# Performance work log

Hardware: AMD Instinct MI355X
Metric: run time of the kernel (lower is better)

Reference implementation:

```python
import jax, jax.numpy as jnp
import numpy as np

N_NODES = 50000
N_EDGES = 800000
N_GRAPHS = 2000
EMB = 300
FEAT = 512
OUT = 256
L = 5


def setup_inputs() -> dict:
    key = jax.random.key(0)
    ks = jax.random.split(key, 24)
    s = 0.05
    inp = {
        "x": jax.random.randint(ks[0], (N_NODES, 2), 0, 3, dtype=jnp.int64 if jax.config.jax_enable_x64 else jnp.int32),
        "edge_index": jax.random.randint(ks[1], (2, N_EDGES), 0, N_NODES),
        "edge_attr": jax.random.randint(ks[2], (N_EDGES, 2), 0, 3),
        "batch": jnp.sort(jax.random.randint(ks[3], (N_NODES,), 0, N_GRAPHS)),
        # node embeddings
        "x_emb1": jax.random.normal(ks[4], (119, EMB), jnp.float32) * s,
        "x_emb2": jax.random.normal(ks[5], (3, EMB), jnp.float32) * s,
        # stacked per-layer GINEConv params [L, ...]
        "edge_e1": jax.random.normal(ks[6], (L, 5, EMB), jnp.float32) * s,
        "edge_e2": jax.random.normal(ks[7], (L, 3, EMB), jnp.float32) * s,
        "W1": jax.random.normal(ks[8], (L, EMB, 2 * EMB), jnp.float32) * s,
        "b1": jnp.zeros((L, 2 * EMB), jnp.float32),
        "W2": jax.random.normal(ks[9], (L, 2 * EMB, EMB), jnp.float32) * s,
        "b2": jnp.zeros((L, EMB), jnp.float32),
        # feat_lin
        "feat_W": jax.random.normal(ks[10], (EMB, FEAT), jnp.float32) * s,
        "feat_b": jnp.zeros((FEAT,), jnp.float32),
        # pred head: Linear(512,256)+ReLU, Linear(256,256)+ReLU, Linear(256,256)
        "p0_W": jax.random.normal(ks[11], (FEAT, FEAT // 2), jnp.float32) * s,
        "p0_b": jnp.zeros((FEAT // 2,), jnp.float32),
        "p1_W": jax.random.normal(ks[12], (FEAT // 2, FEAT // 2), jnp.float32) * s,
        "p1_b": jnp.zeros((FEAT // 2,), jnp.float32),
        "p2_W": jax.random.normal(ks[13], (FEAT // 2, OUT), jnp.float32) * s,
        "p2_b": jnp.zeros((OUT,), jnp.float32),
    }
    return inp


def reference(x, edge_index, edge_attr, batch,
              x_emb1, x_emb2, edge_e1, edge_e2, W1, b1, W2, b2,
              feat_W, feat_b, p0_W, p0_b, p1_W, p1_b, p2_W, p2_b):
    N = x.shape[0]
    # initial node embedding
    h = x_emb1[x[:, 0]] + x_emb2[x[:, 1]]  # [N, EMB]

    # add self loops (appended once; same for every layer)
    loop = jnp.arange(N)
    src = jnp.concatenate([edge_index[0], loop])  # [E+N]
    dst = jnp.concatenate([edge_index[1], loop])
    # self-loop edge_attr = [4, 0]
    ea0 = jnp.concatenate([edge_attr[:, 0], jnp.full((N,), 4, edge_attr.dtype)])
    ea1 = jnp.concatenate([edge_attr[:, 1], jnp.zeros((N,), edge_attr.dtype)])

    for l in range(L):
        ee = edge_e1[l][ea0] + edge_e2[l][ea1]          # [E+N, EMB]
        msg = h[src] + ee                                # gather + add
        aggr = jax.ops.segment_sum(msg, dst, num_segments=N)  # scatter-add
        h = jnp.maximum(aggr @ W1[l] + b1[l], 0.0) @ W2[l] + b2[l]  # GIN MLP
        if l < L - 1:
            h = jnp.maximum(h, 0.0)  # relu (dropout inactive in eval)

    # global mean pool over graphs
    sums = jax.ops.segment_sum(h, batch, num_segments=N_GRAPHS)          # [G, EMB]
    counts = jax.ops.segment_sum(jnp.ones((N,), h.dtype), batch, num_segments=N_GRAPHS)
    hg = sums / jnp.maximum(counts, 1.0)[:, None]

    hg = hg @ feat_W + feat_b                    # feat_lin -> [G, FEAT]
    p = jnp.maximum(hg @ p0_W + p0_b, 0.0)
    p = jnp.maximum(p @ p1_W + p1_b, 0.0)
    proj = p @ p2_W + p2_b                       # [G, OUT]
    return hg, proj
```

## Files before the change

kernel.cpp:

```cpp
#include <hip/hip_runtime.h>
#include <stdint.h>
#include <stddef.h>

typedef unsigned short u16;
typedef __attribute__((ext_vector_type(8))) short short8;
typedef __attribute__((ext_vector_type(4))) float f32x4;

#define N_NODES 50000
#define N_EDGES 800000
#define N_GRAPHS 2000
#define EMB 300
#define EMB_P 320
#define HID 600
#define HID_P 640
#define NP2 384
#define M_P 50176
#define G_P 2048
#define FEAT 512
#define OUTD 256
#define NLAYER 5

#define OFF_EMB1 0
#define N_EMB1   (119 * EMB)
#define OFF_EMB2 (OFF_EMB1 + N_EMB1)
#define N_EMB2   (3 * EMB)
#define OFF_E1   (OFF_EMB2 + N_EMB2)
#define N_E1     (NLAYER * 5 * EMB)
#define OFF_E2   (OFF_E1 + N_E1)
#define N_E2     (NLAYER * 3 * EMB)
#define OFF_W1   (OFF_E2 + N_E2)
#define N_W1     (NLAYER * EMB * HID)
#define OFF_B1   (OFF_W1 + N_W1)
#define N_B1     (NLAYER * HID)
#define OFF_W2   (OFF_B1 + N_B1)
#define N_W2     (NLAYER * HID * EMB)
#define OFF_B2   (OFF_W2 + N_W2)
#define N_B2     (NLAYER * EMB)
#define OFF_FW   (OFF_B2 + N_B2)
#define N_FW     (EMB * FEAT)
#define OFF_FB   (OFF_FW + N_FW)
#define N_FB     (FEAT)
#define OFF_P0W  (OFF_FB + N_FB)
#define N_P0W    (FEAT * (FEAT / 2))
#define OFF_P0B  (OFF_P0W + N_P0W)
#define N_P0B    (FEAT / 2)
#define OFF_P1W  (OFF_P0B + N_P0B)
#define N_P1W    ((FEAT / 2) * (FEAT / 2))
#define OFF_P1B  (OFF_P1W + N_P1W)
#define N_P1B    (FEAT / 2)
#define OFF_P2W  (OFF_P1B + N_P1B)
#define N_P2W    ((FEAT / 2) * OUTD)
#define OFF_P2B  (OFF_P2W + N_P2W)
#define N_P2B    (OUTD)
#define CVT_TOTAL (OFF_P2B + N_P2B)

#define WOFF_W1T 0
#define WN_W1T   (NLAYER * HID_P * EMB_P)
#define WOFF_W2T (WOFF_W1T + WN_W1T)
#define WN_W2T   (NLAYER * NP2 * HID_P)
#define WOFF_FWT (WOFF_W2T + WN_W2T)
#define WN_FWT   (FEAT * EMB_P)
#define WOFF_P0T (WOFF_FWT + WN_FWT)
#define WN_P0T   (OUTD * FEAT)
#define WOFF_P1T (WOFF_P0T + WN_P0T)
#define WN_P1T   (OUTD * OUTD)
#define WOFF_P2T (WOFF_P1T + WN_P1T)
#define WN_P2T   (OUTD * OUTD)
#define WOFF_B1P (WOFF_P2T + WN_P2T)
#define WN_B1P   (NLAYER * HID_P)
#define WOFF_B2P (WOFF_B1P + WN_B1P)
#define WN_B2P   (NLAYER * NP2)
#define W_TOTAL  (WOFF_B2P + WN_B2P)

__device__ __forceinline__ float b2f(u16 u) {
    union { unsigned int i; float f; } c; c.i = ((unsigned int)u) << 16; return c.f;
}
__device__ __forceinline__ u16 f2b(float f) {
    union { float f; unsigned int i; } c; c.f = f;
    unsigned int x = c.i;
    unsigned int lsb = (x >> 16) & 1u;
    x += 0x7fffu + lsb;
    return (u16)(x >> 16);
}
__device__ __forceinline__ int geti(const int* __restrict__ p, long k, int iw) {
    return p[k << iw];
}
__device__ __forceinline__ void gll16(const u16* g, u16* l) {
    __builtin_amdgcn_global_load_lds((const __attribute__((address_space(1))) void*)g,
                                     (__attribute__((address_space(3))) void*)l, 16, 0, 0);
}

__global__ __launch_bounds__(256) void detect_kernel(const void* __restrict__ emb1_raw,
                                                     const int* __restrict__ ei_raw,
                                                     int* __restrict__ flags) {
    __shared__ int cnt_s;
    __shared__ int nz_s;
    int tid = threadIdx.x;
    if (tid == 0) { cnt_s = 0; nz_s = 0; }
    __syncthreads();
    const u16* u = (const u16*)emb1_raw;
    int local = 0;
#pragma unroll
    for (int j = 0; j < 8; j++) {
        u16 w = u[2 * (tid * 8 + j)];
        int e = (w >> 7) & 0xFF;
        if (w == 0 || (e >= 90 && e <= 130)) local++;
    }
    atomicAdd(&cnt_s, local);
    int v = ei_raw[2 * tid + 1];
    if (v != 0) atomicOr(&nz_s, 1);
    __syncthreads();
    if (tid == 0) {
        flags[0] = (cnt_s < 1600) ? 1 : 0;
        flags[1] = nz_s ? 0 : 1;
    }
}

struct CvtArgs { const void* src[16]; };
__constant__ int cvt_off[17] = {OFF_EMB1, OFF_EMB2, OFF_E1, OFF_E2, OFF_W1, OFF_B1,
                                OFF_W2, OFF_B2, OFF_FW, OFF_FB, OFF_P0W, OFF_P0B,
                                OFF_P1W, OFF_P1B, OFF_P2W, OFF_P2B, CVT_TOTAL};

__global__ __launch_bounds__(256) void cvt_all(CvtArgs args, u16* __restrict__ dst,
                                               const int* __restrict__ flags) {
    int idx = blockIdx.x * 256 + threadIdx.x;
    if (idx >= CVT_TOTAL) return;
    int fp32 = flags[0];
    int t = 0;
#pragma unroll
    for (int i = 0; i < 16; i++) {
        if (idx >= cvt_off[i + 1]) t = i + 1;
    }
    int off = idx - cvt_off[t];
    u16 v;
    if (fp32) v = f2b(((const float*)args.src[t])[off]);
    else      v = ((const u16*)args.src[t])[off];
    dst[idx] = v;
}

struct WSeg { int srcOff, Kin, Nin, Kd, Nd, bias; };
__constant__ int wseg_cum[9] = {WOFF_W1T, WOFF_W2T, WOFF_FWT, WOFF_P0T, WOFF_P1T,
                                WOFF_P2T, WOFF_B1P, WOFF_B2P, W_TOTAL};
__constant__ WSeg wsegs[8] = {
    {OFF_W1,  EMB, HID,  EMB_P, HID_P, 0},
    {OFF_W2,  HID, EMB,  HID_P, NP2,   0},
    {OFF_FW,  EMB, FEAT, EMB_P, FEAT,  0},
    {OFF_P0W, FEAT, OUTD, FEAT, OUTD,  0},
    {OFF_P1W, OUTD, OUTD, OUTD, OUTD,  0},
    {OFF_P2W, OUTD, OUTD, OUTD, OUTD,  0},
    {OFF_B1,  HID, 0, 0, HID_P, 1},
    {OFF_B2,  EMB, 0, 0, NP2,   1},
};

__global__ __launch_bounds__(256) void tpad_all(const u16* __restrict__ cbuf,
                                                u16* __restrict__ wbuf) {
    int idx = blockIdx.x * 256 + threadIdx.x;
    if (idx >= W_TOTAL) return;
    int t = 0;
#pragma unroll
    for (int i = 0; i < 8; i++) {
        if (idx >= wseg_cum[i + 1]) t = i + 1;
    }
    WSeg sg = wsegs[t];
    int i = idx - wseg_cum[t];
    u16 v = 0;
    if (sg.bias) {
        int n = i % sg.Nd, l = i / sg.Nd;
        if (n < sg.Kin) v = cbuf[sg.srcOff + l * sg.Kin + n];
    } else {
        int k = i % sg.Kd;
        int r = i / sg.Kd;
        int n = r % sg.Nd, l = r / sg.Nd;
        if (k < sg.Kin && n < sg.Nin) v = cbuf[sg.srcOff + ((long)l * sg.Kin + k) * sg.Nin + n];
    }
    wbuf[idx] = v;
}

__global__ void count_edges(const int* __restrict__ ei, const int* __restrict__ ea,
                            int* __restrict__ deg, int* __restrict__ Ccnt,
                            const int* __restrict__ flags) {
    int e = blockIdx.x * 256 + threadIdx.x;
    if (e >= N_EDGES) return;
    int iw = flags[1];
    int dst = geti(ei, (long)N_EDGES + e, iw);
    if (dst >= 0 && dst < N_NODES) atomicAdd(&deg[dst], 1);
    int a = geti(ea, 2L * e, iw), b = geti(ea, 2L * e + 1, iw);
    if (dst >= 0 && dst < N_NODES && a >= 0 && a < 3 && b >= 0 && b < 3)
        atomicAdd(&Ccnt[dst * 16 + a * 3 + b], 1);
}

__global__ __launch_bounds__(1024) void scan50k(const int* __restrict__ deg,
                                                int* __restrict__ offsets,
                                                int* __restrict__ cursor) {
    __shared__ int buf[1024];
    __shared__ int carry_s;
    int tid = threadIdx.x;
    if (tid == 0) { carry_s = 0; offsets[0] = 0; }
    __syncthreads();
    for (int base = 0; base < N_NODES; base += 1024) {
        int v = (base + tid < N_NODES) ? deg[base + tid] : 0;
        buf[tid] = v;
        __syncthreads();
        for (int off = 1; off < 1024; off <<= 1) {
            int t = (tid >= off) ? buf[tid - off] : 0;
            __syncthreads();
            buf[tid] += t;
            __syncthreads();
        }
        int incl = carry_s + buf[tid];
        if (base + tid < N_NODES) {
            offsets[base + tid + 1] = incl;
            cursor[base + tid] = incl - v;
        }
        __syncthreads();
        if (tid == 0) carry_s += buf[1023];
        __syncthreads();
    }
}

__global__ void fill_csr(const int* __restrict__ ei, int* __restrict__ cursor,
                         int* __restrict__ csr_src, const int* __restrict__ flags) {
    int e = blockIdx.x * 256 + threadIdx.x;
    if (e >= N_EDGES) return;
    int iw = flags[1];
    int src = geti(ei, (long)e, iw);
    int dst = geti(ei, (long)N_EDGES + e, iw);
    if (dst < 0 || dst >= N_NODES) return;
    int pos = atomicAdd(&cursor[dst], 1);
    if (pos >= 0 && pos < N_EDGES) csr_src[pos] = src;
}

__global__ __launch_bounds__(256) void embed_kernel(const int* __restrict__ x,
                                                    const u16* __restrict__ emb1,
                                                    const u16* __restrict__ emb2,
                                                    u16* __restrict__ h,
                                                    const int* __restrict__ flags) {
    int wave = threadIdx.x >> 6, lane = threadIdx.x & 63;
    int n = blockIdx.x * 4 + wave;
    int iw = flags[1];
    int i1 = geti(x, 2L * n, iw), i2 = geti(x, 2L * n + 1, iw);
    i1 = (i1 >= 0 && i1 < 119) ? i1 : 0;
    i2 = (i2 >= 0 && i2 < 3) ? i2 : 0;
#pragma unroll
    for (int j = 0; j < 5; j++) {
        int f = lane + 64 * j;
        float v = 0.f;
        if (f < EMB) v = b2f(emb1[i1 * EMB + f]) + b2f(emb2[i2 * EMB + f]);
        h[(size_t)n * EMB_P + f] = f2b(v);
    }
}

__global__ __launch_bounds__(256) void aggregate_kernel(const u16* __restrict__ h,
                                                        u16* __restrict__ aggr,
                                                        const int* __restrict__ offsets,
                                                        const int* __restrict__ csr_src,
                                                        const int* __restrict__ Ccnt,
                                                        const u16* __restrict__ e1,
                                                        const u16* __restrict__ e2) {
    __shared__ float eetab[15 * EMB_P];
    int tid = threadIdx.x;
    for (int idx = tid; idx < 15 * EMB_P; idx += 256) {
        int c = idx / EMB_P, f = idx % EMB_P;
        float v = 0.f;
        if (f < EMB) v = b2f(e1[(c / 3) * EMB + f]) + b2f(e2[(c % 3) * EMB + f]);
        eetab[idx] = v;
    }
    __syncthreads();
    int wave = tid >> 6, lane = tid & 63;
    int n = blockIdx.x * 4 + wave;
    float acc[5];
#pragma unroll
    for (int j = 0; j < 5; j++) acc[j] = b2f(h[(size_t)n * EMB_P + lane + 64 * j]);
    int e_beg = offsets[n], e_end = offsets[n + 1];
    int cnt = e_end - e_beg;
    if (cnt > 0) {
        int sA = csr_src[e_beg];
        int sB = (cnt > 1) ? csr_src[e_beg + 1] : 0;
        u16 cur[5];
        {
            const u16* hp = h + (size_t)sA * EMB_P + lane;
#pragma unroll
            for (int j = 0; j < 5; j++) cur[j] = hp[64 * j];
        }
        for (int i = 0; i + 1 < cnt; i++) {
            const u16* hq = h + (size_t)sB * EMB_P + lane;
            u16 nxt[5];
#pragma unroll
            for (int j = 0; j < 5; j++) nxt[j] = hq[64 * j];
            int sC = (i + 2 < cnt) ? csr_src[e_beg + i + 2] : 0;
#pragma unroll
            for (int j = 0; j < 5; j++) acc[j] += b2f(cur[j]);
#pragma unroll
            for (int j = 0; j < 5; j++) cur[j] = nxt[j];
            sB = sC;
        }
#pragma unroll
        for (int j = 0; j < 5; j++) acc[j] += b2f(cur[j]);
    }
#pragma unroll
    for (int c = 0; c < 15; c++) {
        float cntf = (float)Ccnt[n * 16 + c] + (c == 12 ? 1.0f : 0.0f);
#pragma unroll
        for (int j = 0; j < 5; j++) acc[j] += cntf * eetab[c * EMB_P + lane + 64 * j];
    }
#pragma unroll
    for (int j = 0; j < 5; j++) aggr[(size_t)n * EMB_P + lane + 64 * j] = f2b(acc[j]);
}

__global__ __launch_bounds__(256) void gemm_bf16(const u16* __restrict__ A,
                                                 const u16* __restrict__ Bt,
                                                 const u16* __restrict__ bias,
                                                 u16* __restrict__ Cb,
                                                 float* __restrict__ Cf,
                                                 int K, int lda, int ldb, int ldc,
                                                 int Mstore, int Nstore, int relu) {
    __shared__ u16 As[128 * 64];
    __shared__ u16 Bs[128 * 64];
    int tid = threadIdx.x;
    int lane = tid & 63, wave = tid >> 6;
    int wm = (wave >> 1) * 64, wn = (wave & 1) * 64;
    int n0 = blockIdx.x * 128, m0 = blockIdx.y * 128;
    int q = lane >> 4, r16 = lane & 15;
    int wrow = wave * 32;
    int lcol = (lane & 7) * 8;

    f32x4 acc[4][4];
#pragma unroll
    for (int i = 0; i < 4; i++)
#pragma unroll
        for (int j = 0; j < 4; j++) acc[i][j] = (f32x4){0.f, 0.f, 0.f, 0.f};

    for (int k0 = 0; k0 < K; k0 += 64) {
#pragma unroll
        for (int p = 0; p < 4; p++) {
            int row = wrow + p * 8 + (lane >> 3);
            gll16(A + (size_t)(m0 + row) * lda + k0 + lcol, &As[(wrow + p * 8) * 64]);
            gll16(Bt + (size_t)(n0 + row) * ldb + k0 + lcol, &Bs[(wrow + p * 8) * 64]);
        }
        __syncthreads();
#pragma unroll
        for (int kk = 0; kk < 2; kk++) {
            short8 af[4], bfr[4];
#pragma unroll
            for (int i = 0; i < 4; i++)
                af[i] = *(const short8*)(&As[(wm + i * 16 + r16) * 64 + kk * 32 + q * 8]);
#pragma unroll
            for (int j = 0; j < 4; j++)
                bfr[j] = *(const short8*)(&Bs[(wn + j * 16 + r16) * 64 + kk * 32 + q * 8]);
#pragma unroll
            for (int i = 0; i < 4; i++)
#pragma unroll
                for (int j = 0; j < 4; j++)
                    acc[i][j] = __builtin_amdgcn_mfma_f32_16x16x32_bf16(af[i], bfr[j], acc[i][j], 0, 0, 0);
        }
        __syncthreads();
    }
#pragma unroll
    for (int i = 0; i < 4; i++) {
#pragma unroll
        for (int j = 0; j < 4; j++) {
            int n_g = n0 + wn + j * 16 + r16;
            float bv = (n_g < Nstore) ? b2f(bias[n_g]) : 0.f;
#pragma unroll
            for (int rr = 0; rr < 4; rr++) {
                int m_g = m0 + wm + i * 16 + q * 4 + rr;
                if (m_g < Mstore && n_g < Nstore) {
                    float v = acc[i][j][rr] + bv;
                    if (relu) v = fmaxf(v, 0.f);
                    if (Cb) Cb[(size_t)m_g * ldc + n_g] = f2b(v);
                    if (Cf) Cf[(size_t)m_g * ldc + n_g] = v;
                }
            }
        }
    }
}

__global__ void graph_bounds(const int* __restrict__ batch, int* __restrict__ gstart,
                             const int* __restrict__ flags) {
    int g = blockIdx.x * 256 + threadIdx.x;
    if (g > N_GRAPHS) return;
    int iw = flags[1];
    int lo = 0, hi = N_NODES;
    while (lo < hi) {
        int mid = (lo + hi) >> 1;
        if (geti(batch, mid, iw) < g) lo = mid + 1; else hi = mid;
    }
    gstart[g] = lo;
}

__global__ __launch_bounds__(256) void pool_kernel(const u16* __restrict__ h,
                                                   const int* __restrict__ gstart,
                                                   u16* __restrict__ hgp) {
    int wave = threadIdx.x >> 6, lane = threadIdx.x & 63;
    int g = blockIdx.x * 4 + wave;
    int s = gstart[g], e = gstart[g + 1];
    float acc[5] = {0.f, 0.f, 0.f, 0.f, 0.f};
    for (int n = s; n < e; n++) {
        const u16* hp = h + (size_t)n * EMB_P + lane;
#pragma unroll
        for (int j = 0; j < 5; j++) acc[j] += b2f(hp[64 * j]);
    }
    int cnt = e - s;
    float inv = 1.0f / (float)(cnt > 1 ? cnt : 1);
#pragma unroll
    for (int j = 0; j < 5; j++) hgp[(size_t)g * EMB_P + lane + 64 * j] = f2b(acc[j] * inv);
}

extern "C" void kernel_launch(void* const* d_in, const int* in_sizes, int n_in,
                              void* d_out, int out_size, void* d_ws, size_t ws_size,
                              hipStream_t stream) {
    const int* x       = (const int*)d_in[0];
    const int* ei      = (const int*)d_in[1];
    const int* ea      = (const int*)d_in[2];
    const int* batch   = (const int*)d_in[3];
    float* out = (float*)d_out;

    char* wp = (char*)d_ws;
    auto alloc = [&](size_t bytes) -> void* {
        void* r = (void*)wp;
        wp += (bytes + 255) & ~(size_t)255;
        return r;
    };
    int* flags   = (int*)alloc(16 * 4);
    int* gstart  = (int*)alloc((N_GRAPHS + 1) * 4);
    int* deg     = (int*)alloc(N_NODES * 4);
    int* cursor  = (int*)alloc(N_NODES * 4);
    int* offsets = (int*)alloc((N_NODES + 1) * 4);
    u16* cbuf    = (u16*)alloc((size_t)CVT_TOTAL * 2);
    u16* wbuf    = (u16*)alloc((size_t)W_TOTAL * 2);
    u16* hg_pre  = (u16*)alloc((size_t)G_P * EMB_P * 2);
    u16* hgbuf   = (u16*)alloc((size_t)G_P * FEAT * 2);
    u16* pbuf0   = (u16*)alloc((size_t)G_P * OUTD * 2);
    u16* pbuf1   = (u16*)alloc((size_t)G_P * OUTD * 2);
    int* csr_src = (int*)alloc(N_EDGES * 4);
    int* Ccnt    = (int*)alloc((size_t)N_NODES * 16 * 4);
    u16* aggr    = (u16*)alloc((size_t)M_P * EMB_P * 2);
    u16* h       = (u16*)alloc((size_t)M_P * EMB_P * 2);

    size_t used = (size_t)(wp - (char*)d_ws);
    size_t remain = (ws_size > used) ? (ws_size - used - 4096) : 0;
    size_t hdnFull = (size_t)M_P * HID_P * 2;
    int nstrip = 8;
    if (remain >= hdnFull)          nstrip = 1;
    else if (remain >= hdnFull / 2) nstrip = 2;
    else if (remain >= hdnFull / 4) nstrip = 4;
    int stripRows = M_P / nstrip;
    u16* hdn = (u16*)alloc(hdnFull / nstrip);

    detect_kernel<<<1, 256, 0, stream>>>(d_in[4], ei, flags);
    CvtArgs ca;
    for (int i = 0; i < 16; i++) ca.src[i] = d_in[4 + i];
    cvt_all<<<(CVT_TOTAL + 255) / 256, 256, 0, stream>>>(ca, cbuf, flags);
    tpad_all<<<(W_TOTAL + 255) / 256, 256, 0, stream>>>(cbuf, wbuf);

    const u16* x_emb1  = cbuf + OFF_EMB1;
    const u16* x_emb2  = cbuf + OFF_EMB2;
    const u16* edge_e1 = cbuf + OFF_E1;
    const u16* edge_e2 = cbuf + OFF_E2;
    const u16* fb      = cbuf + OFF_FB;
    const u16* p0b     = cbuf + OFF_P0B;
    const u16* p1b     = cbuf + OFF_P1B;
    const u16* p2b     = cbuf + OFF_P2B;
    const u16* W1t     = wbuf + WOFF_W1T;
    const u16* W2t     = wbuf + WOFF_W2T;
    const u16* featWt  = wbuf + WOFF_FWT;
    const u16* p0Wt    = wbuf + WOFF_P0T;
    const u16* p1Wt    = wbuf + WOFF_P1T;
    const u16* p2Wt    = wbuf + WOFF_P2T;
    const u16* b1p     = wbuf + WOFF_B1P;
    const u16* b2p     = wbuf + WOFF_B2P;

    hipMemsetAsync(deg, 0, N_NODES * 4, stream);
    hipMemsetAsync(Ccnt, 0, (size_t)N_NODES * 16 * 4, stream);

    count_edges<<<(N_EDGES + 255) / 256, 256, 0, stream>>>(ei, ea, deg, Ccnt, flags);
    scan50k<<<1, 1024, 0, stream>>>(deg, offsets, cursor);
    fill_csr<<<(N_EDGES + 255) / 256, 256, 0, stream>>>(ei, cursor, csr_src, flags);
    graph_bounds<<<(N_GRAPHS + 1 + 255) / 256, 256, 0, stream>>>(batch, gstart, flags);

    embed_kernel<<<N_NODES / 4, 256, 0, stream>>>(x, x_emb1, x_emb2, h, flags);

    for (int l = 0; l < NLAYER; l++) {
        aggregate_kernel<<<N_NODES / 4, 256, 0, stream>>>(
            h, aggr, offsets, csr_src, Ccnt,
            edge_e1 + (size_t)l * 5 * EMB, edge_e2 + (size_t)l * 3 * EMB);
        for (int s = 0; s < nstrip; s++) {
            size_t r0 = (size_t)s * stripRows;
            gemm_bf16<<<dim3(HID_P / 128, stripRows / 128), 256, 0, stream>>>(
                aggr + r0 * EMB_P, W1t + (size_t)l * HID_P * EMB_P,
                b1p + (size_t)l * HID_P, hdn, nullptr,
                EMB_P, EMB_P, EMB_P, HID_P, stripRows, HID_P, 1);
            gemm_bf16<<<dim3(NP2 / 128, stripRows / 128), 256, 0, stream>>>(
                hdn, W2t + (size_t)l * NP2 * HID_P,
                b2p + (size_t)l * NP2, h + r0 * EMB_P, nullptr,
                HID_P, HID_P, HID_P, EMB_P, stripRows, EMB_P, (l < NLAYER - 1) ? 1 : 0);
        }
    }

    pool_kernel<<<N_GRAPHS / 4, 256, 0, stream>>>(h, gstart, hg_pre);

    gemm_bf16<<<dim3(FEAT / 128, G_P / 128), 256, 0, stream>>>(
        hg_pre, featWt, fb, hgbuf, out,
        EMB_P, EMB_P, EMB_P, FEAT, N_GRAPHS, FEAT, 0);
    gemm_bf16<<<dim3(OUTD / 128, G_P / 128), 256, 0, stream>>>(
        hgbuf, p0Wt, p0b, pbuf0, nullptr,
        FEAT, FEAT, FEAT, OUTD, N_GRAPHS, OUTD, 1);
    gemm_bf16<<<dim3(OUTD / 128, G_P / 128), 256, 0, stream>>>(
        pbuf0, p1Wt, p1b, pbuf1, nullptr,
        OUTD, OUTD, OUTD, OUTD, N_GRAPHS, OUTD, 1);
    gemm_bf16<<<dim3(OUTD / 128, G_P / 128), 256, 0, stream>>>(
        pbuf1, p2Wt, p2b, nullptr, out + (size_t)N_GRAPHS * FEAT,
        OUTD, OUTD, OUTD, OUTD, N_GRAPHS, OUTD, 0);
}
```

Measured before the change: 1.628 ms.

## Use 256-row GEMM tiles for GIN MLP and deepen aggregation gather prefetch

Adds a GEMM kernel with 256x128 output tiles, where each wave computes 64x128, and uses it for both GIN MLP matmuls in every layer. Each loaded B tile is reused across more rows, which cuts LDS and global traffic per MFMA. The aggregation loop now keeps two neighbor rows in flight instead of one, to hide gather latency. The costs are higher register pressure from 32 accumulators per wave, lower occupancy, and the strip rows may not divide by 256, which depends on Mstore bounds and on the buffer padding.

```diff
diff --git a/kernel.cpp b/kernel.cpp
--- a/kernel.cpp
+++ b/kernel.cpp
@@ -274,28 +274,53 @@
     int e_beg = offsets[n], e_end = offsets[n + 1];
     int cnt = e_end - e_beg;
     if (cnt > 0) {
-        int sA = csr_src[e_beg];
-        int sB = (cnt > 1) ? csr_src[e_beg + 1] : 0;
-        u16 cur[5];
+        int i0 = csr_src[e_beg];
+        int i1 = (cnt > 1) ? csr_src[e_beg + 1] : 0;
+        int i2 = (cnt > 2) ? csr_src[e_beg + 2] : 0;
+        int i3 = (cnt > 3) ? csr_src[e_beg + 3] : 0;
+        u16 A_[5], B_[5];
         {
-            const u16* hp = h + (size_t)sA * EMB_P + lane;
-#pragma unroll
-            for (int j = 0; j < 5; j++) cur[j] = hp[64 * j];
-        }
-        for (int i = 0; i + 1 < cnt; i++) {
-            const u16* hq = h + (size_t)sB * EMB_P + lane;
-            u16 nxt[5];
-#pragma unroll
-            for (int j = 0; j < 5; j++) nxt[j] = hq[64 * j];
-            int sC = (i + 2 < cnt) ? csr_src[e_beg + i + 2] : 0;
-#pragma unroll
-            for (int j = 0; j < 5; j++) acc[j] += b2f(cur[j]);
-#pragma unroll
-            for (int j = 0; j < 5; j++) cur[j] = nxt[j];
-            sB = sC;
-        }
-#pragma unroll
-        for (int j = 0; j < 5; j++) acc[j] += b2f(cur[j]);
+            const u16* r = h + (size_t)i0 * EMB_P + lane;
+#pragma unroll
+            for (int j = 0; j < 5; j++) A_[j] = r[64 * j];
+        }
+        if (cnt > 1) {
+            const u16* r = h + (size_t)i1 * EMB_P + lane;
+#pragma unroll
+            for (int j = 0; j < 5; j++) B_[j] = r[64 * j];
+        }
+        int e = 0;
+        for (; e + 3 < cnt; e += 2) {
+#pragma unroll
+            for (int j = 0; j < 5; j++) acc[j] += b2f(A_[j]);
+            {
+                const u16* r = h + (size_t)i2 * EMB_P + lane;
+#pragma unroll
+                for (int j = 0; j < 5; j++) A_[j] = r[64 * j];
+            }
+#pragma unroll
+            for (int j = 0; j < 5; j++) acc[j] += b2f(B_[j]);
+            {
+                const u16* r = h + (size_t)i3 * EMB_P + lane;
+#pragma unroll
+                for (int j = 0; j < 5; j++) B_[j] = r[64 * j];
+            }
+            i2 = (e + 4 < cnt) ? csr_src[e_beg + e + 4] : 0;
+            i3 = (e + 5 < cnt) ? csr_src[e_beg + e + 5] : 0;
+        }
+        if (e < cnt) {
+#pragma unroll
+            for (int j = 0; j < 5; j++) acc[j] += b2f(A_[j]);
+        }
+        if (e + 1 < cnt) {
+#pragma unroll
+            for (int j = 0; j < 5; j++) acc[j] += b2f(B_[j]);
+        }
+        if (e + 2 < cnt) {
+            const u16* r = h + (size_t)i2 * EMB_P + lane;
+#pragma unroll
+            for (int j = 0; j < 5; j++) acc[j] += b2f(r[64 * j]);
+        }
     }
 #pragma unroll
     for (int c = 0; c < 15; c++) {
@@ -369,6 +394,76 @@
                     if (relu) v = fmaxf(v, 0.f);
                     if (Cb) Cb[(size_t)m_g * ldc + n_g] = f2b(v);
                     if (Cf) Cf[(size_t)m_g * ldc + n_g] = v;
+                }
+            }
+        }
+    }
+}
+
+__global__ __launch_bounds__(256) void gemm_bf16_256(const u16* __restrict__ A,
+                                                     const u16* __restrict__ Bt,
+                                                     const u16* __restrict__ bias,
+                                                     u16* __restrict__ Cb,
+                                                     int K, int lda, int ldb, int ldc,
+                                                     int Mstore, int Nstore, int relu) {
+    __shared__ u16 As[256 * 64];
+    __shared__ u16 Bs[128 * 64];
+    int tid = threadIdx.x;
+    int lane = tid & 63, wave = tid >> 6;
+    int wm = wave * 64;
+    int n0 = blockIdx.x * 128, m0 = blockIdx.y * 256;
+    int q = lane >> 4, r16 = lane & 15;
+    int lcol = (lane & 7) * 8;
+
+    f32x4 acc[4][8];
+#pragma unroll
+    for (int i = 0; i < 4; i++)
+#pragma unroll
+        for (int j = 0; j < 8; j++) acc[i][j] = (f32x4){0.f, 0.f, 0.f, 0.f};
+
+    for (int k0 = 0; k0 < K; k0 += 64) {
+#pragma unroll
+        for (int p = 0; p < 8; p++) {
+            int row = wm + p * 8 + (lane >> 3);
+            gll16(A + (size_t)(m0 + row) * lda + k0 + lcol, &As[(wm + p * 8) * 64]);
+        }
+#pragma unroll
+        for (int p = 0; p < 4; p++) {
+            int row = wave * 32 + p * 8 + (lane >> 3);
+            gll16(Bt + (size_t)(n0 + row) * ldb + k0 + lcol, &Bs[(wave * 32 + p * 8) * 64]);
+        }
+        __syncthreads();
+#pragma unroll
+        for (int kk = 0; kk < 2; kk++) {
+            short8 af[4], bfr[8];
+#pragma unroll
+            for (int i = 0; i < 4; i++)
+                af[i] = *(const short8*)(&As[(wm + i * 16 + r16) * 64 + kk * 32 + q * 8]);
+#pragma unroll
+            for (int j = 0; j < 8; j++)
+                bfr[j] = *(const short8*)(&Bs[(j * 16 + r16) * 64 + kk * 32 + q * 8]);
+#pragma unroll
+            for (int i = 0; i < 4; i++)
+#pragma unroll
+                for (int j = 0; j < 8; j++)
+                    acc[i][j] = __builtin_amdgcn_mfma_f32_16x16x32_bf16(af[i], bfr[j], acc[i][j], 0, 0, 0);
+        }
+        __syncthreads();
+    }
+#pragma unroll
+    for (int j = 0; j < 8; j++) {
+        int n_g = n0 + j * 16 + r16;
+        if (n_g >= Nstore) continue;
+        float bv = b2f(bias[n_g]);
+#pragma unroll
+        for (int i = 0; i < 4; i++) {
+#pragma unroll
+            for (int rr = 0; rr < 4; rr++) {
+                int m_g = m0 + wm + i * 16 + q * 4 + rr;
+                if (m_g < Mstore) {
+                    float v = acc[i][j][rr] + bv;
+                    if (relu) v = fmaxf(v, 0.f);
+                    Cb[(size_t)m_g * ldc + n_g] = f2b(v);
                 }
             }
         }
@@ -486,13 +581,14 @@
             edge_e1 + (size_t)l * 5 * EMB, edge_e2 + (size_t)l * 3 * EMB);
         for (int s = 0; s < nstrip; s++) {
             size_t r0 = (size_t)s * stripRows;
-            gemm_bf16<<<dim3(HID_P / 128, stripRows / 128), 256, 0, stream>>>(
+            int mtiles = (stripRows + 255) / 256;
+            gemm_bf16_256<<<dim3(HID_P / 128, mtiles), 256, 0, stream>>>(
                 aggr + r0 * EMB_P, W1t + (size_t)l * HID_P * EMB_P,
-                b1p + (size_t)l * HID_P, hdn, nullptr,
+                b1p + (size_t)l * HID_P, hdn,
                 EMB_P, EMB_P, EMB_P, HID_P, stripRows, HID_P, 1);
-            gemm_bf16<<<dim3(NP2 / 128, stripRows / 128), 256, 0, stream>>>(
+            gemm_bf16_256<<<dim3(NP2 / 128, mtiles), 256, 0, stream>>>(
                 hdn, W2t + (size_t)l * NP2 * HID_P,
-                b2p + (size_t)l * NP2, h + r0 * EMB_P, nullptr,
+                b2p + (size_t)l * NP2, h + r0 * EMB_P,
                 HID_P, HID_P, HID_P, EMB_P, stripRows, EMB_P, (l < NLAYER - 1) ? 1 : 0);
         }
     }
```

After: 1.763 ms. 8.3% more time.
